# Kernel tuning notes

Hardware: AMD Instinct MI355X
Metric: run time of the kernel (lower is better)

## Reference

```python
import jax, jax.numpy as jnp
import numpy as np

HIDDEN = 1024
NUM_HEADS = 16
HEAD_DIM = HIDDEN // NUM_HEADS
WINDOW = 512


def setup_inputs() -> dict:
    key = jax.random.key(0)
    ks = jax.random.split(key, 6)
    b, s = 2, 4096
    x = jax.random.normal(ks[0], (b, s, HIDDEN), dtype=jnp.float32)
    attention_mask = jnp.ones((b, s), dtype=jnp.int32)
    scale = 1.0 / np.sqrt(HIDDEN)
    Wq = jax.random.normal(ks[1], (HIDDEN, HIDDEN), dtype=jnp.float32) * scale
    Wk = jax.random.normal(ks[2], (HIDDEN, HIDDEN), dtype=jnp.float32) * scale
    Wv = jax.random.normal(ks[3], (HIDDEN, HIDDEN), dtype=jnp.float32) * scale
    Wo = jax.random.normal(ks[4], (HIDDEN, HIDDEN), dtype=jnp.float32) * scale
    return {"x": x, "attention_mask": attention_mask,
            "Wq": Wq, "Wk": Wk, "Wv": Wv, "Wo": Wo}


def reference(x, attention_mask, Wq, Wk, Wv, Wo):
    b, s, d = x.shape
    # nn.Linear computes x @ W.T
    q = (x @ Wq.T).reshape(b, s, NUM_HEADS, HEAD_DIM).transpose(0, 2, 1, 3)
    k = (x @ Wk.T).reshape(b, s, NUM_HEADS, HEAD_DIM).transpose(0, 2, 1, 3)
    v = (x @ Wv.T).reshape(b, s, NUM_HEADS, HEAD_DIM).transpose(0, 2, 1, 3)
    # [b,h,s,s] scores
    scores = jnp.einsum('bhqd,bhkd->bhqk', q, k) / np.sqrt(HEAD_DIM)
    # causal sliding-window mask: allow j <= i and j >= i - window + 1
    i = jnp.arange(s)[:, None]
    j = jnp.arange(s)[None, :]
    window_mask = (j <= i) & (j >= i - WINDOW + 1)  # [s,s]
    neg_inf = jnp.finfo(scores.dtype).min
    scores = jnp.where(window_mask[None, None], scores, neg_inf)
    pad = attention_mask.astype(bool)[:, None, None, :]  # [b,1,1,s]
    scores = jnp.where(pad, scores, neg_inf)
    probs = jax.nn.softmax(scores, axis=-1)
    out = jnp.einsum('bhqk,bhkd->bhqd', probs, v)
    out = out.transpose(0, 2, 1, 3).reshape(b, s, d)
    return out @ Wo.T
```

## Files before the change

kernel.cpp:

```cpp
#include <hip/hip_runtime.h>
#include <cstdint>
#include <cstddef>

#define HID 1024
#define SEQ 4096
#define NB  2
#define NH  16
#define HD  64
#define WIN 512
#define TOK (NB*SEQ)

typedef _Float16 f16x8 __attribute__((ext_vector_type(8)));
typedef _Float16 f16x4 __attribute__((ext_vector_type(4)));
typedef float    f32x4 __attribute__((ext_vector_type(4)));

__global__ __launch_bounds__(256)
void convert_kernel(const float* __restrict__ X, const float* __restrict__ w0,
                    const float* __restrict__ w1, const float* __restrict__ w2,
                    const float* __restrict__ w3,
                    _Float16* __restrict__ Xh, _Float16* __restrict__ Wh) {
  const int bi = blockIdx.x;
  const float* src; _Float16* dst; size_t off;
  if (bi < 4096) {
    src = X; dst = Xh; off = (size_t)bi * 2048;
  } else {
    const int wi = bi - 4096, z = wi >> 9;
    src = (z == 0) ? w0 : (z == 1) ? w1 : (z == 2) ? w2 : w3;
    dst = Wh + (size_t)z * HID * HID;
    off = (size_t)(wi & 511) * 2048;
  }
  const size_t i = off + (size_t)threadIdx.x * 8;
  f32x4 a = *(const f32x4*)(src + i);
  f32x4 b = *(const f32x4*)(src + i + 4);
  f16x8 o;
#pragma unroll
  for (int r = 0; r < 4; ++r) { o[r] = (_Float16)a[r]; o[r+4] = (_Float16)b[r]; }
  *(f16x8*)(dst + i) = o;
}

__device__ __forceinline__ void gload16(const void* g, void* lds) {
  __builtin_amdgcn_global_load_lds(
      (__attribute__((address_space(1))) void*)(void*)g,
      (__attribute__((address_space(3))) void*)lds, 16, 0, 0);
}

__device__ __forceinline__ void gemm_mainloop(
    const _Float16* __restrict__ A, const _Float16* __restrict__ W,
    _Float16* sA, _Float16* sB, f32x4 (&acc)[4][4], int m0, int n0) {
  const int tid  = threadIdx.x;
  const int lane = tid & 63;
  const int wave = tid >> 6;
  const int wm = wave >> 1, wn = wave & 1;
  const int l15 = lane & 15, quad = lane >> 4;

  const int o0 = tid * 16;
  const int o1 = o0 + 4096;
  const _Float16* a0 = A + (size_t)(m0 + (o0 >> 6)) * HID + ((o0 & 63) >> 1);
  const _Float16* a1 = A + (size_t)(m0 + (o1 >> 6)) * HID + ((o1 & 63) >> 1);
  const _Float16* w0 = W + (size_t)(n0 + (o0 >> 6)) * HID + ((o0 & 63) >> 1);
  const _Float16* w1 = W + (size_t)(n0 + (o1 >> 6)) * HID + ((o1 & 63) >> 1);
  _Float16* la0 = sA + (o0 >> 1);
  _Float16* la1 = sA + (o1 >> 1);
  _Float16* lb0 = sB + (o0 >> 1);
  _Float16* lb1 = sB + (o1 >> 1);

  const int aoff = (wm*64 + l15)*32 + quad*8;
  const int boff = (wn*64 + l15)*32 + quad*8;

  for (int k0 = 0; k0 < HID; k0 += 64) {
    __syncthreads();
    gload16(a0 + k0,      la0);
    gload16(a1 + k0,      la1);
    gload16(a0 + k0 + 32, la0 + 4096);
    gload16(a1 + k0 + 32, la1 + 4096);
    gload16(w0 + k0,      lb0);
    gload16(w1 + k0,      lb1);
    gload16(w0 + k0 + 32, lb0 + 4096);
    gload16(w1 + k0 + 32, lb1 + 4096);
    __syncthreads();
#pragma unroll
    for (int s = 0; s < 2; ++s) {
      const int sb = s * 4096;
      f16x8 af[4], wf[4];
#pragma unroll
      for (int t = 0; t < 4; ++t) {
        af[t] = *(const f16x8*)(sA + sb + aoff + t*512);
        wf[t] = *(const f16x8*)(sB + sb + boff + t*512);
      }
#pragma unroll
      for (int i = 0; i < 4; ++i)
#pragma unroll
        for (int j = 0; j < 4; ++j)
          acc[i][j] = __builtin_amdgcn_mfma_f32_16x16x32_f16(af[i], wf[j], acc[i][j], 0, 0, 0);
    }
  }
}

__global__ __launch_bounds__(256, 3)
void gemm_qkv_kernel(const _Float16* __restrict__ X,
                     const _Float16* __restrict__ Wh,
                     _Float16* __restrict__ Q,
                     _Float16* __restrict__ Kb,
                     _Float16* __restrict__ Vt) {
  __shared__ __align__(16) _Float16 sA[128*64];
  __shared__ __align__(16) _Float16 sB[128*64];
  const int i  = blockIdx.x;
  const int g  = i & 7;
  const int j  = i >> 3;
  const int mi = j & 7;
  const int c  = j >> 3;
  const int z  = c >> 3;
  const int n0 = (c & 7) * 128;
  const int m0 = (g*8 + mi) * 128;
  const _Float16* W = Wh + (size_t)z * HID * HID;
  f32x4 acc[4][4] = {};
  gemm_mainloop(X, W, sA, sB, acc, m0, n0);

  const int tid  = threadIdx.x;
  const int lane = tid & 63;
  const int wave = tid >> 6;
  const int wm = wave >> 1, wn = wave & 1;
  const int l15 = lane & 15, quad = lane >> 4;

  if (z < 2) {
    _Float16* C = (z == 0) ? Q : Kb;
    const float scl = (z == 0) ? 0.18033688011f : 1.0f;
#pragma unroll
    for (int tm = 0; tm < 4; ++tm)
#pragma unroll
      for (int tn = 0; tn < 4; ++tn) {
        const int row = m0 + wm*64 + tm*16 + quad*4;
        const int col = n0 + wn*64 + tn*16 + l15;
#pragma unroll
        for (int r = 0; r < 4; ++r)
          C[(size_t)(row + r)*HID + col] = (_Float16)(acc[tm][tn][r] * scl);
      }
  } else {
#pragma unroll
    for (int tm = 0; tm < 4; ++tm)
#pragma unroll
      for (int tn = 0; tn < 4; ++tn) {
        const int row = m0 + wm*64 + tm*16 + quad*4;
        const int col = n0 + wn*64 + tn*16 + l15;
        f16x4 v;
#pragma unroll
        for (int r = 0; r < 4; ++r) v[r] = (_Float16)acc[tm][tn][r];
        *(f16x4*)(Vt + (size_t)col*TOK + row) = v;
      }
  }
}

__global__ __launch_bounds__(256, 3)
void gemm_o_kernel(const _Float16* __restrict__ A,
                   const _Float16* __restrict__ Wo,
                   float* __restrict__ C) {
  __shared__ __align__(16) _Float16 sA[128*64];
  __shared__ __align__(16) _Float16 sB[128*64];
  const int i  = blockIdx.x;
  const int g  = i & 7;
  const int j  = i >> 3;
  const int mi = j & 7;
  const int n0 = (j >> 3) * 128;
  const int m0 = (g*8 + mi) * 128;
  f32x4 acc[4][4] = {};
  gemm_mainloop(A, Wo, sA, sB, acc, m0, n0);

  const int tid  = threadIdx.x;
  const int lane = tid & 63;
  const int wave = tid >> 6;
  const int wm = wave >> 1, wn = wave & 1;
  const int l15 = lane & 15, quad = lane >> 4;
#pragma unroll
  for (int tm = 0; tm < 4; ++tm)
#pragma unroll
    for (int tn = 0; tn < 4; ++tn) {
      const int row = m0 + wm*64 + tm*16 + quad*4;
      const int col = n0 + wn*64 + tn*16 + l15;
#pragma unroll
      for (int r = 0; r < 4; ++r)
        C[(size_t)(row + r)*HID + col] = acc[tm][tn][r];
    }
}

__global__ __launch_bounds__(512, 4)
void attn_kernel(const _Float16* __restrict__ Q, const _Float16* __restrict__ Kb,
                 const _Float16* __restrict__ Vt, const int* __restrict__ AM,
                 _Float16* __restrict__ O) {
  __shared__ __align__(16) _Float16 sK[128*64];
  __shared__ __align__(16) _Float16 sV[64*128];
  __shared__ __align__(16) _Float16 sP[8*32*64];
  __shared__ int sOK;

  const int bi = blockIdx.x;
  const int g  = bi & 7;
  const int jj = bi >> 3;
  const int combo = g*4 + (jj >> 4);
  const int h = combo & 15, b = combo >> 4;
  const int qb = jj & 15;

  const int tid  = threadIdx.x;
  const int lane = tid & 63, wave = tid >> 6;
  const int l15 = lane & 15, quad = lane >> 4;

  const int q0 = qb * 256;
  const int qw = q0 + wave * 32;

  const int swz = l15 & 7;
  const int cA8 = ((quad ^ swz) << 3);
  const int cB8 = (((quad + 4) ^ swz) << 3);

  f16x8 qf[2][2];
#pragma unroll
  for (int ns = 0; ns < 2; ++ns) {
    const size_t qbse = (size_t)(b*SEQ + qw + ns*16 + l15)*HID + h*HD + quad*8;
    qf[ns][0] = *(const f16x8*)(Q + qbse);
    qf[ns][1] = *(const f16x8*)(Q + qbse + 32);
  }

  int stage_lo = (q0 - (WIN - 1));
  stage_lo = (stage_lo < 0) ? 0 : (stage_lo & ~127);
  const int nst = (q0 + 256 - stage_lo) >> 7;

  if (tid == 0) sOK = 1;
  __syncthreads();
  {
    int ok = 1;
    for (int j = stage_lo + tid; j < q0 + 256; j += 512) ok &= (AM[b*SEQ + j] != 0);
    if (!ok) sOK = 0;
  }
  __syncthreads();
  const bool allok = (sOK != 0);

  const int prow = tid >> 3;
  const int pc   = tid & 7;
  const int pco  = ((pc ^ (prow & 7)) << 3);
  f16x8 pk0, pk1, pv0, pv1;
  {
    const _Float16* kp = Kb + (size_t)(b*SEQ + stage_lo + prow)*HID + h*HD + pco;
    pk0 = *(const f16x8*)kp;
    pk1 = *(const f16x8*)(kp + (size_t)64*HID);
    const _Float16* vp = Vt + (size_t)(h*HD + prow)*TOK + b*SEQ + stage_lo + pco;
    pv0 = *(const f16x8*)vp;
    pv1 = *(const f16x8*)(vp + 64);
  }

  float l_run[2] = {0.0f, 0.0f};
  f32x4 o[4][2] = {};
  _Float16* myP = sP + wave * (32*64);

  for (int st = 0; st < nst; ++st) {
    const int j0st = stage_lo + st*128;
    __syncthreads();
    *(f16x8*)(sK + prow*64 + pc*8)        = pk0;
    *(f16x8*)(sK + (64 + prow)*64 + pc*8) = pk1;
    *(f16x8*)(sV + prow*128 + pc*8)       = pv0;
    *(f16x8*)(sV + prow*128 + 64 + pc*8)  = pv1;
    __syncthreads();
    if (st + 1 < nst) {
      const int jn = j0st + 128;
      const _Float16* kp = Kb + (size_t)(b*SEQ + jn + prow)*HID + h*HD + pco;
      pk0 = *(const f16x8*)kp;
      pk1 = *(const f16x8*)(kp + (size_t)64*HID);
      const _Float16* vp = Vt + (size_t)(h*HD + prow)*TOK + b*SEQ + jn + pco;
      pv0 = *(const f16x8*)vp;
      pv1 = *(const f16x8*)(vp + 64);
    }

#pragma unroll
    for (int s = 0; s < 2; ++s) {
      const int j0 = j0st + s*64;
      if (j0 > qw + 31 || j0 + 63 < qw - (WIN - 1)) continue;
      const bool interior = (j0 + 63 <= qw) && (j0 >= qw - (WIN - 32));

#pragma unroll
      for (int ns = 0; ns < 2; ++ns) {
        f32x4 sc[4];
#pragma unroll
        for (int t = 0; t < 4; ++t) {
          const f16x8 kf0 = *(const f16x8*)(sK + (s*64 + t*16 + l15)*64 + cA8);
          const f16x8 kf1 = *(const f16x8*)(sK + (s*64 + t*16 + l15)*64 + cB8);
          f32x4 a = {};
          a = __builtin_amdgcn_mfma_f32_16x16x32_f16(kf0, qf[ns][0], a, 0, 0, 0);
          a = __builtin_amdgcn_mfma_f32_16x16x32_f16(kf1, qf[ns][1], a, 0, 0, 0);
          sc[t] = a;
        }

        if (!allok) {
#pragma unroll
          for (int t = 0; t < 4; ++t)
#pragma unroll
            for (int r = 0; r < 4; ++r) {
              const float ad = (AM[b*SEQ + j0 + t*16 + quad*4 + r] == 0) ? -2e30f : 0.0f;
              sc[t][r] += ad;
            }
        }
        if (!interior) {
          const int i = qw + ns*16 + l15;
#pragma unroll
          for (int t = 0; t < 4; ++t)
#pragma unroll
            for (int r = 0; r < 4; ++r) {
              const int j = j0 + t*16 + quad*4 + r;
              const bool valid = (unsigned)(i - j) < WIN;
              sc[t][r] = valid ? sc[t][r] : -1e30f;
            }
        }
        float sum = 0.0f;
#pragma unroll
        for (int t = 0; t < 4; ++t) {
          f16x4 pvv;
#pragma unroll
          for (int r = 0; r < 4; ++r) {
            const float p = __builtin_amdgcn_exp2f(sc[t][r]);
            sum += p;
            pvv[r] = (_Float16)p;
          }
          const int paddr = (ns*16 + l15)*64 + (((2*t + (quad >> 1)) ^ swz) << 3) + (quad & 1)*4;
          *(f16x4*)(myP + paddr) = pvv;
        }
        sum += __shfl_xor(sum, 16, 64);
        sum += __shfl_xor(sum, 32, 64);
        l_run[ns] += sum;
      }

      const f16x8 pf00 = *(const f16x8*)(myP + l15*64 + cA8);
      const f16x8 pf01 = *(const f16x8*)(myP + l15*64 + cB8);
      const f16x8 pf10 = *(const f16x8*)(myP + (16 + l15)*64 + cA8);
      const f16x8 pf11 = *(const f16x8*)(myP + (16 + l15)*64 + cB8);
#pragma unroll
      for (int dt = 0; dt < 4; ++dt) {
        const f16x8 vf0 = *(const f16x8*)(sV + (dt*16 + l15)*128 + s*64 + cA8);
        const f16x8 vf1 = *(const f16x8*)(sV + (dt*16 + l15)*128 + s*64 + cB8);
        o[dt][0] = __builtin_amdgcn_mfma_f32_16x16x32_f16(vf0, pf00, o[dt][0], 0, 0, 0);
        o[dt][0] = __builtin_amdgcn_mfma_f32_16x16x32_f16(vf1, pf01, o[dt][0], 0, 0, 0);
        o[dt][1] = __builtin_amdgcn_mfma_f32_16x16x32_f16(vf0, pf10, o[dt][1], 0, 0, 0);
        o[dt][1] = __builtin_amdgcn_mfma_f32_16x16x32_f16(vf1, pf11, o[dt][1], 0, 0, 0);
      }
    }
  }

  const float inv[2] = {1.0f / fmaxf(l_run[0], 1e-30f), 1.0f / fmaxf(l_run[1], 1e-30f)};
#pragma unroll
  for (int ns = 0; ns < 2; ++ns) {
    const size_t ob = (size_t)(b*SEQ + qw + ns*16 + l15)*HID + h*HD + quad*4;
#pragma unroll
    for (int dt = 0; dt < 4; ++dt) {
      f16x4 v;
#pragma unroll
      for (int r = 0; r < 4; ++r) v[r] = (_Float16)(o[dt][ns][r] * inv[ns]);
      *(f16x4*)(O + ob + dt*16) = v;
    }
  }
}

extern "C" void kernel_launch(void* const* d_in, const int* in_sizes, int n_in,
                              void* d_out, int out_size, void* d_ws, size_t ws_size,
                              hipStream_t stream) {
  const float* X  = (const float*)d_in[0];
  const int*   AM = (const int*)d_in[1];
  const float* Wq = (const float*)d_in[2];
  const float* Wk = (const float*)d_in[3];
  const float* Wv = (const float*)d_in[4];
  const float* Wo = (const float*)d_in[5];
  float* out = (float*)d_out;

  _Float16* Xh = (_Float16*)d_ws;
  _Float16* Wh = Xh + (size_t)TOK*HID;
  _Float16* Qb = Wh + (size_t)4*HID*HID;
  _Float16* Kb = Qb + (size_t)TOK*HID;
  _Float16* Vt = Kb + (size_t)TOK*HID;
  _Float16* AO = Vt + (size_t)TOK*HID;

  convert_kernel<<<dim3(4096 + 4*512), dim3(256), 0, stream>>>(X, Wq, Wk, Wv, Wo, Xh, Wh);
  gemm_qkv_kernel<<<dim3(1536), dim3(256), 0, stream>>>(Xh, Wh, Qb, Kb, Vt);
  attn_kernel<<<dim3(512), dim3(512), 0, stream>>>(Qb, Kb, Vt, AM, AO);
  gemm_o_kernel<<<dim3(512), dim3(256), 0, stream>>>(AO, Wh + (size_t)3*HID*HID, out);
}
```

Before: 236.7 us.

## Halve attention query tile per block and per wave, doubling grid size

The attention kernel now gives each block 128 queries (16 per wave) instead of 256 (32 per wave), and launches 1024 blocks instead of 512. The P tile becomes 16x32 per wave with a new swizzle, and the PV product is split into two 32-key halves. The mask pre-check is reduced with a wave-level __all vote, which removes two block barriers. The goal is better occupancy and CU balance with fewer registers, at the cost of restaging K/V more often per query, since the 512-key window overhead is amortised over fewer queries.

New measurement: 218.6 us. -7.6%, faster.

```diff
diff --git a/kernel.cpp b/kernel.cpp
--- a/kernel.cpp
+++ b/kernel.cpp
@@ -188,48 +188,40 @@
                  _Float16* __restrict__ O) {
   __shared__ __align__(16) _Float16 sK[128*64];
   __shared__ __align__(16) _Float16 sV[64*128];
-  __shared__ __align__(16) _Float16 sP[8*32*64];
-  __shared__ int sOK;
+  __shared__ __align__(16) _Float16 sP[8*16*32];
 
   const int bi = blockIdx.x;
   const int g  = bi & 7;
   const int jj = bi >> 3;
-  const int combo = g*4 + (jj >> 4);
+  const int combo = g*4 + (jj >> 5);
   const int h = combo & 15, b = combo >> 4;
-  const int qb = jj & 15;
+  const int qb = jj & 31;
 
   const int tid  = threadIdx.x;
   const int lane = tid & 63, wave = tid >> 6;
   const int l15 = lane & 15, quad = lane >> 4;
 
-  const int q0 = qb * 256;
-  const int qw = q0 + wave * 32;
+  const int q0 = qb * 128;
+  const int qw = q0 + wave * 16;
 
   const int swz = l15 & 7;
   const int cA8 = ((quad ^ swz) << 3);
   const int cB8 = (((quad + 4) ^ swz) << 3);
 
-  f16x8 qf[2][2];
-#pragma unroll
-  for (int ns = 0; ns < 2; ++ns) {
-    const size_t qbse = (size_t)(b*SEQ + qw + ns*16 + l15)*HID + h*HD + quad*8;
-    qf[ns][0] = *(const f16x8*)(Q + qbse);
-    qf[ns][1] = *(const f16x8*)(Q + qbse + 32);
+  f16x8 qf0, qf1;
+  {
+    const size_t qbse = (size_t)(b*SEQ + qw + l15)*HID + h*HD + quad*8;
+    qf0 = *(const f16x8*)(Q + qbse);
+    qf1 = *(const f16x8*)(Q + qbse + 32);
   }
 
   int stage_lo = (q0 - (WIN - 1));
   stage_lo = (stage_lo < 0) ? 0 : (stage_lo & ~127);
-  const int nst = (q0 + 256 - stage_lo) >> 7;
-
-  if (tid == 0) sOK = 1;
-  __syncthreads();
-  {
-    int ok = 1;
-    for (int j = stage_lo + tid; j < q0 + 256; j += 512) ok &= (AM[b*SEQ + j] != 0);
-    if (!ok) sOK = 0;
-  }
-  __syncthreads();
-  const bool allok = (sOK != 0);
+  const int nst = (q0 + 128 - stage_lo) >> 7;
+
+  int okv = 1;
+  for (int j = stage_lo + lane; j < q0 + 128; j += 64) okv &= (AM[b*SEQ + j] != 0);
+  const bool allok = (__all(okv) != 0);
 
   const int prow = tid >> 3;
   const int pc   = tid & 7;
@@ -244,9 +236,9 @@
     pv1 = *(const f16x8*)(vp + 64);
   }
 
-  float l_run[2] = {0.0f, 0.0f};
-  f32x4 o[4][2] = {};
-  _Float16* myP = sP + wave * (32*64);
+  float l_run = 0.0f;
+  f32x4 o[4] = {};
+  _Float16* myP = sP + wave * (16*32);
 
   for (int st = 0; st < nst; ++st) {
     const int j0st = stage_lo + st*128;
@@ -269,45 +261,47 @@
 #pragma unroll
     for (int s = 0; s < 2; ++s) {
       const int j0 = j0st + s*64;
-      if (j0 > qw + 31 || j0 + 63 < qw - (WIN - 1)) continue;
-      const bool interior = (j0 + 63 <= qw) && (j0 >= qw - (WIN - 32));
-
-#pragma unroll
-      for (int ns = 0; ns < 2; ++ns) {
-        f32x4 sc[4];
-#pragma unroll
-        for (int t = 0; t < 4; ++t) {
-          const f16x8 kf0 = *(const f16x8*)(sK + (s*64 + t*16 + l15)*64 + cA8);
-          const f16x8 kf1 = *(const f16x8*)(sK + (s*64 + t*16 + l15)*64 + cB8);
-          f32x4 a = {};
-          a = __builtin_amdgcn_mfma_f32_16x16x32_f16(kf0, qf[ns][0], a, 0, 0, 0);
-          a = __builtin_amdgcn_mfma_f32_16x16x32_f16(kf1, qf[ns][1], a, 0, 0, 0);
-          sc[t] = a;
-        }
-
-        if (!allok) {
-#pragma unroll
-          for (int t = 0; t < 4; ++t)
-#pragma unroll
-            for (int r = 0; r < 4; ++r) {
-              const float ad = (AM[b*SEQ + j0 + t*16 + quad*4 + r] == 0) ? -2e30f : 0.0f;
-              sc[t][r] += ad;
-            }
-        }
-        if (!interior) {
-          const int i = qw + ns*16 + l15;
-#pragma unroll
-          for (int t = 0; t < 4; ++t)
-#pragma unroll
-            for (int r = 0; r < 4; ++r) {
-              const int j = j0 + t*16 + quad*4 + r;
-              const bool valid = (unsigned)(i - j) < WIN;
-              sc[t][r] = valid ? sc[t][r] : -1e30f;
-            }
-        }
-        float sum = 0.0f;
-#pragma unroll
-        for (int t = 0; t < 4; ++t) {
+      if (j0 > qw + 15 || j0 + 63 < qw - (WIN - 1)) continue;
+      const bool interior = (j0 + 63 <= qw) && (j0 >= qw - (WIN - 16));
+
+      f32x4 sc[4];
+#pragma unroll
+      for (int t = 0; t < 4; ++t) {
+        const f16x8 kf0 = *(const f16x8*)(sK + (s*64 + t*16 + l15)*64 + cA8);
+        const f16x8 kf1 = *(const f16x8*)(sK + (s*64 + t*16 + l15)*64 + cB8);
+        f32x4 a = {};
+        a = __builtin_amdgcn_mfma_f32_16x16x32_f16(kf0, qf0, a, 0, 0, 0);
+        a = __builtin_amdgcn_mfma_f32_16x16x32_f16(kf1, qf1, a, 0, 0, 0);
+        sc[t] = a;
+      }
+
+      if (!allok) {
+#pragma unroll
+        for (int t = 0; t < 4; ++t)
+#pragma unroll
+          for (int r = 0; r < 4; ++r) {
+            const float ad = (AM[b*SEQ + j0 + t*16 + quad*4 + r] == 0) ? -2e30f : 0.0f;
+            sc[t][r] += ad;
+          }
+      }
+      if (!interior) {
+        const int i = qw + l15;
+#pragma unroll
+        for (int t = 0; t < 4; ++t)
+#pragma unroll
+          for (int r = 0; r < 4; ++r) {
+            const int j = j0 + t*16 + quad*4 + r;
+            const bool valid = (unsigned)(i - j) < WIN;
+            sc[t][r] = valid ? sc[t][r] : -1e30f;
+          }
+      }
+
+      float sum = 0.0f;
+#pragma unroll
+      for (int kh = 0; kh < 2; ++kh) {
+#pragma unroll
+        for (int u = 0; u < 2; ++u) {
+          const int t = 2*kh + u;
           f16x4 pvv;
 #pragma unroll
           for (int r = 0; r < 4; ++r) {
@@ -315,41 +309,31 @@
             sum += p;
             pvv[r] = (_Float16)p;
           }
-          const int paddr = (ns*16 + l15)*64 + (((2*t + (quad >> 1)) ^ swz) << 3) + (quad & 1)*4;
-          *(f16x4*)(myP + paddr) = pvv;
+          const int pch = (2*u + (quad >> 1)) ^ (l15 & 3);
+          *(f16x4*)(myP + l15*32 + pch*8 + (quad & 1)*4) = pvv;
         }
-        sum += __shfl_xor(sum, 16, 64);
-        sum += __shfl_xor(sum, 32, 64);
-        l_run[ns] += sum;
-      }
-
-      const f16x8 pf00 = *(const f16x8*)(myP + l15*64 + cA8);
-      const f16x8 pf01 = *(const f16x8*)(myP + l15*64 + cB8);
-      const f16x8 pf10 = *(const f16x8*)(myP + (16 + l15)*64 + cA8);
-      const f16x8 pf11 = *(const f16x8*)(myP + (16 + l15)*64 + cB8);
-#pragma unroll
-      for (int dt = 0; dt < 4; ++dt) {
-        const f16x8 vf0 = *(const f16x8*)(sV + (dt*16 + l15)*128 + s*64 + cA8);
-        const f16x8 vf1 = *(const f16x8*)(sV + (dt*16 + l15)*128 + s*64 + cB8);
-        o[dt][0] = __builtin_amdgcn_mfma_f32_16x16x32_f16(vf0, pf00, o[dt][0], 0, 0, 0);
-        o[dt][0] = __builtin_amdgcn_mfma_f32_16x16x32_f16(vf1, pf01, o[dt][0], 0, 0, 0);
-        o[dt][1] = __builtin_amdgcn_mfma_f32_16x16x32_f16(vf0, pf10, o[dt][1], 0, 0, 0);
-        o[dt][1] = __builtin_amdgcn_mfma_f32_16x16x32_f16(vf1, pf11, o[dt][1], 0, 0, 0);
-      }
+        const f16x8 pf = *(const f16x8*)(myP + l15*32 + ((quad ^ (l15 & 3)) << 3));
+#pragma unroll
+        for (int dt = 0; dt < 4; ++dt) {
+          const f16x8 vf = *(const f16x8*)(sV + (dt*16 + l15)*128 + s*64 +
+                                           (((kh*4 + quad) ^ swz) << 3));
+          o[dt] = __builtin_amdgcn_mfma_f32_16x16x32_f16(vf, pf, o[dt], 0, 0, 0);
+        }
+      }
+      sum += __shfl_xor(sum, 16, 64);
+      sum += __shfl_xor(sum, 32, 64);
+      l_run += sum;
     }
   }
 
-  const float inv[2] = {1.0f / fmaxf(l_run[0], 1e-30f), 1.0f / fmaxf(l_run[1], 1e-30f)};
-#pragma unroll
-  for (int ns = 0; ns < 2; ++ns) {
-    const size_t ob = (size_t)(b*SEQ + qw + ns*16 + l15)*HID + h*HD + quad*4;
-#pragma unroll
-    for (int dt = 0; dt < 4; ++dt) {
-      f16x4 v;
-#pragma unroll
-      for (int r = 0; r < 4; ++r) v[r] = (_Float16)(o[dt][ns][r] * inv[ns]);
-      *(f16x4*)(O + ob + dt*16) = v;
-    }
+  const float inv = 1.0f / fmaxf(l_run, 1e-30f);
+  const size_t ob = (size_t)(b*SEQ + qw + l15)*HID + h*HD + quad*4;
+#pragma unroll
+  for (int dt = 0; dt < 4; ++dt) {
+    f16x4 v;
+#pragma unroll
+    for (int r = 0; r < 4; ++r) v[r] = (_Float16)(o[dt][r] * inv);
+    *(f16x4*)(O + ob + dt*16) = v;
   }
 }
 
@@ -373,6 +357,6 @@
 
   convert_kernel<<<dim3(4096 + 4*512), dim3(256), 0, stream>>>(X, Wq, Wk, Wv, Wo, Xh, Wh);
   gemm_qkv_kernel<<<dim3(1536), dim3(256), 0, stream>>>(Xh, Wh, Qb, Kb, Vt);
-  attn_kernel<<<dim3(512), dim3(512), 0, stream>>>(Qb, Kb, Vt, AM, AO);
+  attn_kernel<<<dim3(1024), dim3(512), 0, stream>>>(Qb, Kb, Vt, AM, AO);
   gemm_o_kernel<<<dim3(512), dim3(256), 0, stream>>>(AO, Wh + (size_t)3*HID*HID, out);
 }
```
